# Kernel tuning notes

Measured on AMD Instinct MI355X. Metric: run time of the kernel, lower is better.

## Reference

```python
import jax, jax.numpy as jnp
import numpy as np

B, O, K, GS = 4096, 11008, 4096, 128  # batch, out_features, in_features, group_size
G = K // GS  # num groups = 32


def _unpack_int4(packed):
    """packed: [N, K//2] int values in [0,256) holding two 4-bit nibbles (low first).
    Returns signed int4 values as float32 [N, K]."""
    low = packed & 15
    high = (packed >> 4) & 15
    q = jnp.stack([low, high], axis=-1).reshape(packed.shape[0], -1)  # interleave low,high
    return jnp.where(q >= 8, q - 16, q).astype(jnp.float32)


def setup_inputs() -> dict:
    key = jax.random.key(0)
    k1, k2, k3, k4, k5 = jax.random.split(key, 5)
    x = jax.random.randint(k1, (B, K // 2), 0, 256, dtype=jnp.int32)
    a_scale = jax.random.uniform(k2, (B, G), dtype=jnp.float32).astype(jnp.float16)
    w_packed = jax.random.randint(k3, (O, K // 2), 0, 256, dtype=jnp.int32)
    w_scale = jax.random.uniform(k4, (O, G), dtype=jnp.float32).astype(jnp.float16)
    bias = (jax.random.normal(k5, (O,), dtype=jnp.float32) * 0.02).astype(jnp.float16)
    return {"x": x, "a_scale": a_scale, "w_packed": w_packed, "w_scale": w_scale,
            "bias": bias, "group_size": GS}


def reference(x, a_scale, w_packed, w_scale, bias, group_size):
    # out[b,o] = sum_g a_scale[b,g] * w_scale[o,g] * sum_{k in g} x_int4[b,k] * w_int4[o,k] + bias[o]
    # Fold the per-group scales into the dequantized operands, then a single GEMM
    # (mathematically identical to group-wise int accumulate + dequant).
    b, o = x.shape[0], w_packed.shape[0]
    k = x.shape[1] * 2
    g = k // group_size
    xq = _unpack_int4(x).reshape(b, g, group_size) * a_scale.astype(jnp.float32)[:, :, None]
    wq = _unpack_int4(w_packed).reshape(o, g, group_size) * w_scale.astype(jnp.float32)[:, :, None]
    out = jnp.einsum('bgk,ogk->bo', xq, wq).astype(jnp.float16)  # [B, O] fp16
    return out + bias
```

## Files before the change

kernel.cpp:

```cpp
#include <hip/hip_runtime.h>


#define B_DIM 4096
#define O_DIM 11008
#define K_DIM 4096
#define G_NUM 32

#define NX32 8388608u
#define NW32 22544384u
#define X8_BYTES  16777216u
#define W8_BYTES  45088768u

typedef int   i32x4 __attribute__((ext_vector_type(4)));
typedef float f32x4 __attribute__((ext_vector_type(4)));

__device__ __forceinline__ unsigned pack2(int v) {
    int t = v ^ 0x88;
    unsigned lo = (unsigned)(((t & 15) - 8) & 0xFF);
    unsigned hi = (unsigned)((((t >> 4) & 15) - 8) & 0xFF);
    return lo | (hi << 8);
}

__global__ __launch_bounds__(256)
void unpack_kernel(const int* __restrict__ xq, const int* __restrict__ wq,
                   unsigned char* __restrict__ X8, unsigned char* __restrict__ W8) {
    unsigned t = blockIdx.x * 256u + threadIdx.x;
    const int* src;
    unsigned char* dst;
    if (t < NX32 / 8) {
        src = xq + (size_t)t * 8;
        dst = X8 + (size_t)t * 16;
    } else {
        unsigned j = t - NX32 / 8;
        src = wq + (size_t)j * 8;
        dst = W8 + (size_t)j * 16;
    }
    int4 v0 = ((const int4*)src)[0];
    int4 v1 = ((const int4*)src)[1];
    uint4 o;
    o.x = pack2(v0.x) | (pack2(v0.y) << 16);
    o.y = pack2(v0.z) | (pack2(v0.w) << 16);
    o.z = pack2(v1.x) | (pack2(v1.y) << 16);
    o.w = pack2(v1.z) | (pack2(v1.w) << 16);
    *(uint4*)dst = o;
}

__global__ __launch_bounds__(256)
void tscale_kernel(const float* __restrict__ as_, const float* __restrict__ ws_,
                   float* __restrict__ asT, float* __restrict__ wsT) {
    __shared__ float tile[64][33];
    const int blk = blockIdx.x, t = threadIdx.x;
    const float* src; float* dst; int R0, RTOT;
    if (blk < 64) { src = as_; dst = asT; R0 = blk * 64;        RTOT = B_DIM; }
    else          { src = ws_; dst = wsT; R0 = (blk - 64) * 64; RTOT = O_DIM; }
    {
        const int r = t >> 2, cc = (t & 3) * 8;
        const float* p = src + (size_t)(R0 + r) * G_NUM + cc;
        f32x4 v0 = *(const f32x4*)p;
        f32x4 v1 = *(const f32x4*)(p + 4);
#pragma unroll
        for (int k = 0; k < 4; ++k) { tile[r][cc + k] = v0[k]; tile[r][cc + 4 + k] = v1[k]; }
    }
    __syncthreads();
    {
        const int g = t >> 3, bc = (t & 7) * 8;
        f32x4 w0, w1;
#pragma unroll
        for (int k = 0; k < 4; ++k) { w0[k] = tile[bc + k][g]; w1[k] = tile[bc + 4 + k][g]; }
        float* q = dst + (size_t)g * RTOT + R0 + bc;
        *(f32x4*)q = w0;
        *(f32x4*)(q + 4) = w1;
    }
}

__global__ __launch_bounds__(256, 2)
void gemm_i8(const unsigned char* __restrict__ X8, const unsigned char* __restrict__ W8,
             const float* __restrict__ asT, const float* __restrict__ wsT,
             const float* __restrict__ bias, float* __restrict__ out) {
    __shared__ __align__(16) unsigned char A0[16384];
    __shared__ __align__(16) unsigned char B0[16384];
    __shared__ __align__(16) unsigned char A1[16384];
    __shared__ __align__(16) unsigned char B1[16384];

    const int tid  = threadIdx.x;
    const int wv   = tid >> 6;
    const int lane = tid & 63;
    const int quad = lane >> 4;
    const int lq   = lane & 15;
    const int bm   = blockIdx.x;
    const int bn   = blockIdx.y;
    const int wm   = (wv & 1) << 6;
    const int wn   = (wv >> 1) << 6;

    f32x4 facc[4][4] = {};

    const int l8 = lane >> 3;
    const int c8 = lane & 7;
    const int sw_chunk = ((c8 ^ l8) << 4);
    const size_t xrow0 = (size_t)(bm * 128) * K_DIM;
    const size_t wrow0 = (size_t)(bn * 128) * K_DIM;
    const int abase = bm * 128 + wm + (quad << 2);
    const int wbase = bn * 128 + wn + lq;
    const int pa0 = ((quad ^ (lq & 7)) << 4);
    const int pa1 = (((4 + quad) ^ (lq & 7)) << 4);

    auto stage = [&](int g, unsigned char* Ad, unsigned char* Bd) {
        const int gb = g << 7;
#pragma unroll
        for (int s = 0; s < 4; ++s) {
            const int slab = (wv << 2) + s;
            const int row  = (slab << 3) + l8;
            const unsigned char* gpA = X8 + xrow0 + (size_t)row * K_DIM + gb + sw_chunk;
            const unsigned char* gpB = W8 + wrow0 + (size_t)row * K_DIM + gb + sw_chunk;
            __builtin_amdgcn_global_load_lds(
                (const __attribute__((address_space(1))) void*)gpA,
                (__attribute__((address_space(3))) void*)(Ad + (slab << 10)), 16, 0, 0);
            __builtin_amdgcn_global_load_lds(
                (const __attribute__((address_space(1))) void*)gpB,
                (__attribute__((address_space(3))) void*)(Bd + (slab << 10)), 16, 0, 0);
        }
    };

    auto compute = [&](int g, const unsigned char* Ab, const unsigned char* Bb) {
        f32x4 asr[4];
        float wsn[4];
#pragma unroll
        for (int i = 0; i < 4; ++i)
            asr[i] = *(const f32x4*)&asT[(g << 12) + abase + (i << 4)];
#pragma unroll
        for (int j = 0; j < 4; ++j)
            wsn[j] = wsT[(size_t)g * O_DIM + wbase + (j << 4)];

        i32x4 bv0[4], bv1[4];
#pragma unroll
        for (int j = 0; j < 4; ++j) {
            bv0[j] = *(const i32x4*)&Bb[((wn + (j << 4) + lq) << 7) + pa0];
            bv1[j] = *(const i32x4*)&Bb[((wn + (j << 4) + lq) << 7) + pa1];
        }
        i32x4 a0c = *(const i32x4*)&Ab[((wm + lq) << 7) + pa0];
        i32x4 a1c = *(const i32x4*)&Ab[((wm + lq) << 7) + pa1];

#pragma unroll
        for (int i = 0; i < 4; ++i) {
            const i32x4 a0 = a0c, a1 = a1c;
            if (i < 3) {
                a0c = *(const i32x4*)&Ab[((wm + ((i + 1) << 4) + lq) << 7) + pa0];
                a1c = *(const i32x4*)&Ab[((wm + ((i + 1) << 4) + lq) << 7) + pa1];
            }
            i32x4 q[4];
#pragma unroll
            for (int j = 0; j < 4; ++j)
                q[j] = __builtin_amdgcn_mfma_i32_16x16x64_i8(a0, bv0[j], (i32x4){0, 0, 0, 0}, 0, 0, 0);
#pragma unroll
            for (int j = 0; j < 4; ++j)
                q[j] = __builtin_amdgcn_mfma_i32_16x16x64_i8(a1, bv1[j], q[j], 0, 0, 0);
#pragma unroll
            for (int j = 0; j < 4; ++j) {
                const f32x4 s = asr[i] * wsn[j];
                f32x4 gf;
#pragma unroll
                for (int r = 0; r < 4; ++r) gf[r] = (float)q[j][r];
                facc[i][j] += gf * s;
            }
        }
    };

    stage(0, A0, B0);

    for (int g2 = 0; g2 < G_NUM; g2 += 2) {
        __syncthreads();
        stage(g2 + 1, A1, B1);
        compute(g2, A0, B0);

        __syncthreads();
        if (g2 + 2 < G_NUM) stage(g2 + 2, A0, B0);
        compute(g2 + 1, A1, B1);
    }

    const int n0 = bn * 128 + wn + lq;
    const int m0 = bm * 128 + wm + (quad << 2);
    float bvs[4];
#pragma unroll
    for (int j = 0; j < 4; ++j) bvs[j] = bias[n0 + (j << 4)];
#pragma unroll
    for (int i = 0; i < 4; ++i) {
#pragma unroll
        for (int r = 0; r < 4; ++r) {
            float* orow = out + (size_t)(m0 + (i << 4) + r) * O_DIM;
#pragma unroll
            for (int j = 0; j < 4; ++j)
                orow[n0 + (j << 4)] = facc[i][j][r] + bvs[j];
        }
    }
}

extern "C" void kernel_launch(void* const* d_in, const int* in_sizes, int n_in,
                              void* d_out, int out_size, void* d_ws, size_t ws_size,
                              hipStream_t stream) {
    const int*   xq   = (const int*)d_in[0];
    const float* as_  = (const float*)d_in[1];
    const int*   wq   = (const int*)d_in[2];
    const float* ws_  = (const float*)d_in[3];
    const float* bias = (const float*)d_in[4];
    float* out        = (float*)d_out;

    unsigned char* X8 = (unsigned char*)d_ws;
    unsigned char* W8 = X8 + X8_BYTES;
    float* asT = (float*)((unsigned char*)d_ws + X8_BYTES + W8_BYTES);
    float* wsT = asT + (size_t)G_NUM * B_DIM;

    unpack_kernel<<<(NX32 + NW32) / 8 / 256, 256, 0, stream>>>(xq, wq, X8, W8);
    tscale_kernel<<<64 + 172, 256, 0, stream>>>(as_, ws_, asT, wsT);
    gemm_i8<<<dim3(B_DIM / 128, O_DIM / 128), 256, 0, stream>>>(X8, W8, asT, wsT, bias, out);
}
```

Before: 523.9 us.

## Software-pipeline MFMA with rescale using double-buffered int accumulators and sched barriers

```diff
diff --git a/kernel.cpp b/kernel.cpp
--- a/kernel.cpp
+++ b/kernel.cpp
@@ -13,6 +13,13 @@
 
 typedef int   i32x4 __attribute__((ext_vector_type(4)));
 typedef float f32x4 __attribute__((ext_vector_type(4)));
+typedef float f32x2 __attribute__((ext_vector_type(2)));
+
+#define GLOAD16(src, dst) __builtin_amdgcn_global_load_lds(                      \
+    (const __attribute__((address_space(1))) void*)(src),                        \
+    (__attribute__((address_space(3))) void*)(dst), 16, 0, 0)
+
+#define SGB(mask, n) __builtin_amdgcn_sched_group_barrier((mask), (n), 0)
 
 __device__ __forceinline__ unsigned pack2(int v) {
     int t = v ^ 0x88;
@@ -92,7 +99,8 @@
     const int wm   = (wv & 1) << 6;
     const int wn   = (wv >> 1) << 6;
 
-    f32x4 facc[4][4] = {};
+    f32x2 facc[4][4][2] = {};
+    const i32x4 Z = {0, 0, 0, 0};
 
     const int l8 = lane >> 3;
     const int c8 = lane & 7;
@@ -110,14 +118,8 @@
         for (int s = 0; s < 4; ++s) {
             const int slab = (wv << 2) + s;
             const int row  = (slab << 3) + l8;
-            const unsigned char* gpA = X8 + xrow0 + (size_t)row * K_DIM + gb + sw_chunk;
-            const unsigned char* gpB = W8 + wrow0 + (size_t)row * K_DIM + gb + sw_chunk;
-            __builtin_amdgcn_global_load_lds(
-                (const __attribute__((address_space(1))) void*)gpA,
-                (__attribute__((address_space(3))) void*)(Ad + (slab << 10)), 16, 0, 0);
-            __builtin_amdgcn_global_load_lds(
-                (const __attribute__((address_space(1))) void*)gpB,
-                (__attribute__((address_space(3))) void*)(Bd + (slab << 10)), 16, 0, 0);
+            GLOAD16(X8 + xrow0 + (size_t)row * K_DIM + gb + sw_chunk, Ad + (slab << 10));
+            GLOAD16(W8 + wrow0 + (size_t)row * K_DIM + gb + sw_chunk, Bd + (slab << 10));
         }
     };
 
@@ -137,32 +139,77 @@
             bv0[j] = *(const i32x4*)&Bb[((wn + (j << 4) + lq) << 7) + pa0];
             bv1[j] = *(const i32x4*)&Bb[((wn + (j << 4) + lq) << 7) + pa1];
         }
-        i32x4 a0c = *(const i32x4*)&Ab[((wm + lq) << 7) + pa0];
-        i32x4 a1c = *(const i32x4*)&Ab[((wm + lq) << 7) + pa1];
-
-#pragma unroll
-        for (int i = 0; i < 4; ++i) {
-            const i32x4 a0 = a0c, a1 = a1c;
-            if (i < 3) {
-                a0c = *(const i32x4*)&Ab[((wm + ((i + 1) << 4) + lq) << 7) + pa0];
-                a1c = *(const i32x4*)&Ab[((wm + ((i + 1) << 4) + lq) << 7) + pa1];
-            }
-            i32x4 q[4];
+
+        i32x4 qA[4], qB[4];
+
+        auto resc = [&](int i, const i32x4 (&q)[4]) {
 #pragma unroll
             for (int j = 0; j < 4; ++j)
-                q[j] = __builtin_amdgcn_mfma_i32_16x16x64_i8(a0, bv0[j], (i32x4){0, 0, 0, 0}, 0, 0, 0);
-#pragma unroll
-            for (int j = 0; j < 4; ++j)
-                q[j] = __builtin_amdgcn_mfma_i32_16x16x64_i8(a1, bv1[j], q[j], 0, 0, 0);
-#pragma unroll
-            for (int j = 0; j < 4; ++j) {
-                const f32x4 s = asr[i] * wsn[j];
-                f32x4 gf;
-#pragma unroll
-                for (int r = 0; r < 4; ++r) gf[r] = (float)q[j][r];
-                facc[i][j] += gf * s;
-            }
-        }
+#pragma unroll
+                for (int p = 0; p < 2; ++p) {
+                    f32x2 d;
+                    d[0] = (float)q[j][(p << 1)];
+                    d[1] = (float)q[j][(p << 1) + 1];
+                    f32x2 sa;
+                    sa[0] = asr[i][(p << 1)];
+                    sa[1] = asr[i][(p << 1) + 1];
+                    const f32x2 s = sa * wsn[j];
+                    facc[i][j][p] += s * d;
+                }
+        };
+
+        i32x4 a0_0 = *(const i32x4*)&Ab[((wm +  0 + lq) << 7) + pa0];
+        i32x4 a1_0 = *(const i32x4*)&Ab[((wm +  0 + lq) << 7) + pa1];
+        i32x4 a0_1 = *(const i32x4*)&Ab[((wm + 16 + lq) << 7) + pa0];
+        i32x4 a1_1 = *(const i32x4*)&Ab[((wm + 16 + lq) << 7) + pa1];
+
+#pragma unroll
+        for (int j = 0; j < 4; ++j)
+            qA[j] = __builtin_amdgcn_mfma_i32_16x16x64_i8(a0_0, bv0[j], Z, 0, 0, 0);
+#pragma unroll
+        for (int j = 0; j < 4; ++j)
+            qA[j] = __builtin_amdgcn_mfma_i32_16x16x64_i8(a1_0, bv1[j], qA[j], 0, 0, 0);
+        i32x4 a0_2 = *(const i32x4*)&Ab[((wm + 32 + lq) << 7) + pa0];
+        i32x4 a1_2 = *(const i32x4*)&Ab[((wm + 32 + lq) << 7) + pa1];
+        SGB(0x100, 12);
+#pragma unroll
+        for (int k = 0; k < 8; ++k) SGB(0x8, 1);
+
+#pragma unroll
+        for (int j = 0; j < 4; ++j)
+            qB[j] = __builtin_amdgcn_mfma_i32_16x16x64_i8(a0_1, bv0[j], Z, 0, 0, 0);
+#pragma unroll
+        for (int j = 0; j < 4; ++j)
+            qB[j] = __builtin_amdgcn_mfma_i32_16x16x64_i8(a1_1, bv1[j], qB[j], 0, 0, 0);
+        resc(0, qA);
+        i32x4 a0_3 = *(const i32x4*)&Ab[((wm + 48 + lq) << 7) + pa0];
+        i32x4 a1_3 = *(const i32x4*)&Ab[((wm + 48 + lq) << 7) + pa1];
+        SGB(0x100, 2);
+#pragma unroll
+        for (int k = 0; k < 8; ++k) { SGB(0x8, 1); SGB(0x2, 4); }
+
+#pragma unroll
+        for (int j = 0; j < 4; ++j)
+            qA[j] = __builtin_amdgcn_mfma_i32_16x16x64_i8(a0_2, bv0[j], Z, 0, 0, 0);
+#pragma unroll
+        for (int j = 0; j < 4; ++j)
+            qA[j] = __builtin_amdgcn_mfma_i32_16x16x64_i8(a1_2, bv1[j], qA[j], 0, 0, 0);
+        resc(1, qB);
+        SGB(0x100, 2);
+#pragma unroll
+        for (int k = 0; k < 8; ++k) { SGB(0x8, 1); SGB(0x2, 4); }
+
+#pragma unroll
+        for (int j = 0; j < 4; ++j)
+            qB[j] = __builtin_amdgcn_mfma_i32_16x16x64_i8(a0_3, bv0[j], Z, 0, 0, 0);
+#pragma unroll
+        for (int j = 0; j < 4; ++j)
+            qB[j] = __builtin_amdgcn_mfma_i32_16x16x64_i8(a1_3, bv1[j], qB[j], 0, 0, 0);
+        resc(2, qA);
+#pragma unroll
+        for (int k = 0; k < 8; ++k) { SGB(0x8, 1); SGB(0x2, 4); }
+
+        resc(3, qB);
     };
 
     stage(0, A0, B0);
@@ -185,12 +232,15 @@
 #pragma unroll
     for (int i = 0; i < 4; ++i) {
 #pragma unroll
-        for (int r = 0; r < 4; ++r) {
-            float* orow = out + (size_t)(m0 + (i << 4) + r) * O_DIM;
-#pragma unroll
-            for (int j = 0; j < 4; ++j)
-                orow[n0 + (j << 4)] = facc[i][j][r] + bvs[j];
-        }
+        for (int p = 0; p < 2; ++p)
+#pragma unroll
+            for (int e = 0; e < 2; ++e) {
+                const int r = (p << 1) + e;
+                float* orow = out + (size_t)(m0 + (i << 4) + r) * O_DIM;
+#pragma unroll
+                for (int j = 0; j < 4; ++j)
+                    orow[n0 + (j << 4)] = facc[i][j][p][e] + bvs[j];
+            }
     }
 }
 
```

Result: no change. 524.2 us (+0.1%).
